# Kernel tuning notes

Measured on AMD Instinct MI355X. Metric: run time of the kernel, lower is better.

## Reference

```python
import jax, jax.numpy as jnp
import numpy as np

COLOR_SIZE = 4
SIZE = 64
FILTERS = 512
LENGTH = SIZE * SIZE * 3  # 12288


def setup_inputs() -> dict:
    key = jax.random.key(0)
    k1, k2, k3 = jax.random.split(key, 3)
    example = jax.random.randint(k1, (8, SIZE, SIZE, 3), 0, COLOR_SIZE, dtype=jnp.int32)
    kernel = jax.random.normal(k2, (FILTERS, LENGTH), dtype=jnp.float32)
    bias = jnp.zeros((FILTERS,), dtype=jnp.float32)
    dense_w = jax.random.normal(k3, (FILTERS, COLOR_SIZE), dtype=jnp.float32) * 0.02
    dense_b = jnp.zeros((COLOR_SIZE,), dtype=jnp.float32)
    return {"example": example, "kernel": kernel, "bias": bias,
            "dense_w": dense_w, "dense_b": dense_b}


def reference(example, kernel, bias, dense_w, dense_b):
    B = example.shape[0]
    L = kernel.shape[1]  # 12288
    # normalize int pixels to [-1, 1)
    x = example.astype(jnp.float32) / COLOR_SIZE * 2.0 - 1.0
    x = x.reshape(B, L)                                   # [B, L]
    # FFT-based long (causal full) convolution, fft_length = 2L
    Xf = jnp.fft.rfft(x, n=2 * L, axis=-1)                # [B, L+1] complex64
    Kf = jnp.fft.rfft(kernel, n=2 * L, axis=-1)           # [F, L+1]
    y = jnp.fft.irfft(Xf[:, None, :] * Kf[None, :, :], n=2 * L, axis=-1)[..., :L]  # [B, F, L]
    y = jnp.transpose(y, (0, 2, 1)) + bias                # [B, L, F]
    y = jax.nn.relu(y)
    out = y @ dense_w + dense_b                           # [B, L, color_size]
    return out.reshape(B, SIZE, SIZE, 3, COLOR_SIZE).astype(jnp.float32)
```

## Files before the change

### kernel.cpp

```cpp
#include <hip/hip_runtime.h>

#define FF 512
#define LL 12288
#define NJC 1556
#define NR 128

typedef _Float16 half8 __attribute__((ext_vector_type(8)));
typedef float    f32x4 __attribute__((ext_vector_type(4)));

__global__ __launch_bounds__(256) void build_At(const float* __restrict__ kern,
                                                _Float16* __restrict__ At) {
    int tid  = blockIdx.x * 256 + threadIdx.x;
    int lane = tid & 63;
    int rest = tid >> 6;
    int dc   = rest % 384;
    int ft   = rest / 384;
    int f    = ft * 16 + (lane & 15);
    int d0   = dc * 32 + (lane >> 4) * 8;
    const float* src = kern + (size_t)f * LL + d0;
    half8 v;
#pragma unroll
    for (int i = 0; i < 8; ++i) v[i] = (_Float16)src[i];
    ((half8*)At)[tid] = v;
}

__global__ __launch_bounds__(256) void build_XB(const int* __restrict__ ex,
                                                _Float16* __restrict__ XB) {
    int tid = blockIdx.x * 256 + threadIdx.x;
    if (tid >= NJC * NR) return;
    int r  = tid & 127;
    int jc = tid >> 7;
    int s  = r >> 3, b = r & 7;
    int j0 = jc * 8;
    half8 v;
#pragma unroll
    for (int i = 0; i < 8; ++i) {
        int idx = LL - 1 - (j0 + i) - s;
        float x = 0.f;
        if (idx >= 0) x = (float)ex[b * LL + idx] * 0.5f - 1.0f;
        v[i] = (_Float16)x;
    }
    ((half8*)XB)[tid] = v;
}

__global__ __launch_bounds__(256) void init_out(const float* __restrict__ db,
                                                float* __restrict__ out) {
    int tid = blockIdx.x * 256 + threadIdx.x;
    out[tid] = db[tid & 3];
}

__device__ __forceinline__ void gl_lds16(const half8* g, half8* l) {
    __builtin_amdgcn_global_load_lds((const __attribute__((address_space(1))) void*)g,
                                     (__attribute__((address_space(3))) void*)l, 16, 0, 0);
}

__global__ __launch_bounds__(256, 2) void conv_main(const _Float16* __restrict__ At,
                                                    const _Float16* __restrict__ XB,
                                                    const float* __restrict__ bias,
                                                    const float* __restrict__ dw,
                                                    float* __restrict__ out) {
    __shared__ half8 Abuf[2][4][8][64];

    int bx    = blockIdx.x;
    int slot  = bx & 7;
    int f_blk = slot >> 1;
    int n_blk = 383 - ((bx >> 3) * 2 + (slot & 1));
    int n0 = n_blk << 5;
    int M  = (n_blk + 4) >> 2;

    int tid  = threadIdx.x;
    int lane = tid & 63;
    int wid  = tid >> 6;
    int quad = lane >> 4;
    int bb   = lane & 7;
    int nh   = (lane >> 3) & 1;

    const half8* Ag  = (const half8*)At;
    const half8* ag0 = Ag + ((size_t)(f_blk * 8 + wid) * 384) * 64 + lane;
    const half8* ag1 = Ag + ((size_t)(f_blk * 8 + wid + 4) * 384) * 64 + lane;

    const half8* Bg = (const half8*)XB;
    int jc0 = 1534 - 4 * n_blk + quad - 2 * nh;
    const half8* pB[4];
#pragma unroll
    for (int t = 0; t < 4; ++t) {
        int tt = wid * 4 + t;
        int r  = (15 - tt) * 8 + bb;
        pB[t] = Bg + (size_t)jc0 * 128 + r;
    }

    f32x4 acc[8][4];
#pragma unroll
    for (int r8 = 0; r8 < 8; ++r8)
#pragma unroll
        for (int t = 0; t < 4; ++t) acc[r8][t] = (f32x4){0.f, 0.f, 0.f, 0.f};

#pragma unroll
    for (int sub = 0; sub < 4; ++sub) {
        gl_lds16(ag0 + (size_t)sub * 64, &Abuf[0][sub][wid][lane]);
        gl_lds16(ag1 + (size_t)sub * 64, &Abuf[0][sub][wid + 4][lane]);
    }
    half8 bcur[4], bnxt[4];
#pragma unroll
    for (int t = 0; t < 4; ++t) bcur[t] = pB[t][0];
    __syncthreads();

    for (int mc = 0; mc < M; ++mc) {
        int buf = mc & 1;
        if (mc + 1 < M) {
            size_t oa = (size_t)(mc + 1) * 256;
#pragma unroll
            for (int sub = 0; sub < 4; ++sub) {
                gl_lds16(ag0 + oa + (size_t)sub * 64, &Abuf[buf ^ 1][sub][wid][lane]);
                gl_lds16(ag1 + oa + (size_t)sub * 64, &Abuf[buf ^ 1][sub][wid + 4][lane]);
            }
        }
#pragma unroll
        for (int sub = 0; sub < 4; ++sub) {
            int dc = mc * 4 + sub;
            size_t ob = (size_t)(dc + 1) * 512;
#pragma unroll
            for (int t = 0; t < 4; ++t) bnxt[t] = pB[t][ob];
            half8 a[8];
#pragma unroll
            for (int r8 = 0; r8 < 8; ++r8) a[r8] = Abuf[buf][sub][r8][lane];
#pragma unroll
            for (int r8 = 0; r8 < 8; ++r8)
#pragma unroll
                for (int t = 0; t < 4; ++t)
                    acc[r8][t] = __builtin_amdgcn_mfma_f32_16x16x32_f16(a[r8], bcur[t], acc[r8][t], 0, 0, 0);
#pragma unroll
            for (int t = 0; t < 4; ++t) bcur[t] = bnxt[t];
        }
        __syncthreads();
    }

    float p[4][4] = {{0.f}};
#pragma unroll
    for (int r8 = 0; r8 < 8; ++r8) {
#pragma unroll
        for (int reg = 0; reg < 4; ++reg) {
            int f = f_blk * 128 + r8 * 16 + quad * 4 + reg;
            float bs = bias[f];
            float4 w = *(const float4*)(dw + (size_t)f * 4);
#pragma unroll
            for (int t = 0; t < 4; ++t) {
                float y = fmaxf(acc[r8][t][reg] + bs, 0.f);
                p[t][0] += y * w.x; p[t][1] += y * w.y;
                p[t][2] += y * w.z; p[t][3] += y * w.w;
            }
        }
    }
#pragma unroll
    for (int t = 0; t < 4; ++t)
#pragma unroll
        for (int c = 0; c < 4; ++c) {
            float v = p[t][c];
            v += __shfl_xor(v, 16, 64);
            v += __shfl_xor(v, 32, 64);
            p[t][c] = v;
        }
    if (quad == 0) {
#pragma unroll
        for (int t = 0; t < 4; ++t) {
            int n = n0 + (wid * 4 + t) + 16 * nh;
            float* o = out + ((size_t)bb * LL + n) * 4;
#pragma unroll
            for (int c = 0; c < 4; ++c) atomicAdd(o + c, p[t][c]);
        }
    }
}

extern "C" void kernel_launch(void* const* d_in, const int* in_sizes, int n_in,
                              void* d_out, int out_size, void* d_ws, size_t ws_size,
                              hipStream_t stream) {
    const int*   ex   = (const int*)d_in[0];
    const float* kern = (const float*)d_in[1];
    const float* bias = (const float*)d_in[2];
    const float* dw   = (const float*)d_in[3];
    const float* db   = (const float*)d_in[4];
    float* out = (float*)d_out;

    _Float16* At = (_Float16*)d_ws;
    _Float16* XB = (_Float16*)((char*)d_ws + (size_t)FF * LL * 2);

    hipLaunchKernelGGL(build_At, dim3(3072), dim3(256), 0, stream, kern, At);
    hipLaunchKernelGGL(build_XB, dim3(778),  dim3(256), 0, stream, ex, XB);
    hipLaunchKernelGGL(init_out, dim3(1536), dim3(256), 0, stream, db, out);
    hipLaunchKernelGGL(conv_main, dim3(1536), dim3(256), 0, stream, At, XB, bias, dw, out);
}
```

Measured before the change: 520.1 us.

## Switch causal-conv GEMM from 16x16x32 to 32x32x16 MFMA tiles

Changes the main Toeplitz-style convolution GEMM to use 32x32x16 f16 MFMA instructions instead of 16x16x32. The A-operand layout produced by build_At, the LDS buffer shape, the B fragment indexing and the epilogue row mapping are all reworked to match the new fragment layout. The aim is fewer MFMA issues and operand fetches per FLOP and better register-level reuse of each A/B fragment. It raises accumulator register pressure (16 floats per tile) and changes the B load pattern, which could affect occupancy or memory coalescing.

```diff
diff --git a/kernel.cpp b/kernel.cpp
--- a/kernel.cpp
+++ b/kernel.cpp
@@ -5,18 +5,18 @@
 #define NJC 1556
 #define NR 128
 
-typedef _Float16 half8 __attribute__((ext_vector_type(8)));
-typedef float    f32x4 __attribute__((ext_vector_type(4)));
+typedef _Float16 half8  __attribute__((ext_vector_type(8)));
+typedef float    f32x16 __attribute__((ext_vector_type(16)));
 
 __global__ __launch_bounds__(256) void build_At(const float* __restrict__ kern,
                                                 _Float16* __restrict__ At) {
     int tid  = blockIdx.x * 256 + threadIdx.x;
     int lane = tid & 63;
     int rest = tid >> 6;
-    int dc   = rest % 384;
-    int ft   = rest / 384;
-    int f    = ft * 16 + (lane & 15);
-    int d0   = dc * 32 + (lane >> 4) * 8;
+    int kc   = rest % 768;
+    int ft   = rest / 768;
+    int f    = ft * 32 + (lane & 31);
+    int d0   = kc * 16 + (lane >> 5) * 8;
     const float* src = kern + (size_t)f * LL + d0;
     half8 v;
 #pragma unroll
@@ -59,114 +59,126 @@
                                                     const float* __restrict__ bias,
                                                     const float* __restrict__ dw,
                                                     float* __restrict__ out) {
-    __shared__ half8 Abuf[2][4][8][64];
+    __shared__ half8 Abuf[2][8][4][64];
 
     int bx    = blockIdx.x;
     int slot  = bx & 7;
     int f_blk = slot >> 1;
     int n_blk = 383 - ((bx >> 3) * 2 + (slot & 1));
     int n0 = n_blk << 5;
-    int M  = (n_blk + 4) >> 2;
+    int S  = n_blk + 1;
+    int M  = (S + 3) >> 2;
 
     int tid  = threadIdx.x;
     int lane = tid & 63;
     int wid  = tid >> 6;
-    int quad = lane >> 4;
+    int kh   = lane >> 5;
     int bb   = lane & 7;
-    int nh   = (lane >> 3) & 1;
-
-    const half8* Ag  = (const half8*)At;
-    const half8* ag0 = Ag + ((size_t)(f_blk * 8 + wid) * 384) * 64 + lane;
-    const half8* ag1 = Ag + ((size_t)(f_blk * 8 + wid + 4) * 384) * 64 + lane;
+    int nh   = (lane >> 3) & 3;
+
+    const half8* Ag = (const half8*)At;
+    const half8* ag = Ag + ((size_t)(f_blk * 4 + wid) * 768) * 64 + lane;
 
     const half8* Bg = (const half8*)XB;
-    int jc0 = 1534 - 4 * n_blk + quad - 2 * nh;
-    const half8* pB[4];
-#pragma unroll
-    for (int t = 0; t < 4; ++t) {
-        int tt = wid * 4 + t;
-        int r  = (15 - tt) * 8 + bb;
-        pB[t] = Bg + (size_t)jc0 * 128 + r;
-    }
-
-    f32x4 acc[8][4];
-#pragma unroll
-    for (int r8 = 0; r8 < 8; ++r8)
-#pragma unroll
-        for (int t = 0; t < 4; ++t) acc[r8][t] = (f32x4){0.f, 0.f, 0.f, 0.f};
-
-#pragma unroll
-    for (int sub = 0; sub < 4; ++sub) {
-        gl_lds16(ag0 + (size_t)sub * 64, &Abuf[0][sub][wid][lane]);
-        gl_lds16(ag1 + (size_t)sub * 64, &Abuf[0][sub][wid + 4][lane]);
-    }
-    half8 bcur[4], bnxt[4];
-#pragma unroll
-    for (int t = 0; t < 4; ++t) bcur[t] = pB[t][0];
+    const half8* pB[2];
+#pragma unroll
+    for (int ti = 0; ti < 2; ++ti) {
+        int n_base = n0 + (wid * 2 + ti) * 4;
+        int Qt = LL - 1 - n_base - nh;
+        int s  = Qt & 7;
+        int jc0 = Qt >> 3;
+        pB[ti] = Bg + (size_t)(jc0 + kh) * 128 + s * 8 + bb;
+    }
+
+    f32x16 acc[4][2];
+#pragma unroll
+    for (int mt = 0; mt < 4; ++mt)
+#pragma unroll
+        for (int ti = 0; ti < 2; ++ti)
+#pragma unroll
+            for (int r = 0; r < 16; ++r) acc[mt][ti][r] = 0.f;
+
+#pragma unroll
+    for (int kc = 0; kc < 8; ++kc)
+        gl_lds16(ag + (size_t)kc * 64, &Abuf[0][kc][wid][lane]);
+    half8 bf[2][2][2];
+#pragma unroll
+    for (int ti = 0; ti < 2; ++ti) {
+        bf[0][0][ti] = pB[ti][0];
+        bf[0][1][ti] = pB[ti][256];
+    }
     __syncthreads();
 
     for (int mc = 0; mc < M; ++mc) {
         int buf = mc & 1;
         if (mc + 1 < M) {
-            size_t oa = (size_t)(mc + 1) * 256;
-#pragma unroll
-            for (int sub = 0; sub < 4; ++sub) {
-                gl_lds16(ag0 + oa + (size_t)sub * 64, &Abuf[buf ^ 1][sub][wid][lane]);
-                gl_lds16(ag1 + oa + (size_t)sub * 64, &Abuf[buf ^ 1][sub][wid + 4][lane]);
+            size_t oa = (size_t)(mc + 1) * 512;
+#pragma unroll
+            for (int kc = 0; kc < 8; ++kc)
+                gl_lds16(ag + oa + (size_t)kc * 64, &Abuf[buf ^ 1][kc][wid][lane]);
+        }
+#pragma unroll
+        for (int d4 = 0; d4 < 4; ++d4) {
+            int dcg = mc * 4 + d4;
+            int p   = dcg & 1;
+            size_t ob = (size_t)(dcg + 1) * 512;
+#pragma unroll
+            for (int ti = 0; ti < 2; ++ti) {
+                bf[p ^ 1][0][ti] = pB[ti][ob];
+                bf[p ^ 1][1][ti] = pB[ti][ob + 256];
             }
-        }
-#pragma unroll
-        for (int sub = 0; sub < 4; ++sub) {
-            int dc = mc * 4 + sub;
-            size_t ob = (size_t)(dc + 1) * 512;
-#pragma unroll
-            for (int t = 0; t < 4; ++t) bnxt[t] = pB[t][ob];
-            half8 a[8];
-#pragma unroll
-            for (int r8 = 0; r8 < 8; ++r8) a[r8] = Abuf[buf][sub][r8][lane];
-#pragma unroll
-            for (int r8 = 0; r8 < 8; ++r8)
-#pragma unroll
-                for (int t = 0; t < 4; ++t)
-                    acc[r8][t] = __builtin_amdgcn_mfma_f32_16x16x32_f16(a[r8], bcur[t], acc[r8][t], 0, 0, 0);
-#pragma unroll
-            for (int t = 0; t < 4; ++t) bcur[t] = bnxt[t];
+            half8 a0[4], a1[4];
+#pragma unroll
+            for (int mt = 0; mt < 4; ++mt) {
+                a0[mt] = Abuf[buf][d4 * 2][mt][lane];
+                a1[mt] = Abuf[buf][d4 * 2 + 1][mt][lane];
+            }
+#pragma unroll
+            for (int mt = 0; mt < 4; ++mt)
+#pragma unroll
+                for (int ti = 0; ti < 2; ++ti)
+                    acc[mt][ti] = __builtin_amdgcn_mfma_f32_32x32x16_f16(a0[mt], bf[p][0][ti], acc[mt][ti], 0, 0, 0);
+#pragma unroll
+            for (int mt = 0; mt < 4; ++mt)
+#pragma unroll
+                for (int ti = 0; ti < 2; ++ti)
+                    acc[mt][ti] = __builtin_amdgcn_mfma_f32_32x32x16_f16(a1[mt], bf[p][1][ti], acc[mt][ti], 0, 0, 0);
         }
         __syncthreads();
     }
 
-    float p[4][4] = {{0.f}};
-#pragma unroll
-    for (int r8 = 0; r8 < 8; ++r8) {
-#pragma unroll
-        for (int reg = 0; reg < 4; ++reg) {
-            int f = f_blk * 128 + r8 * 16 + quad * 4 + reg;
+    float p[2][4] = {{0.f}};
+#pragma unroll
+    for (int mt = 0; mt < 4; ++mt) {
+#pragma unroll
+        for (int reg = 0; reg < 16; ++reg) {
+            int row = (reg & 3) + 8 * (reg >> 2) + 4 * kh;
+            int f   = f_blk * 128 + mt * 32 + row;
             float bs = bias[f];
             float4 w = *(const float4*)(dw + (size_t)f * 4);
 #pragma unroll
-            for (int t = 0; t < 4; ++t) {
-                float y = fmaxf(acc[r8][t][reg] + bs, 0.f);
-                p[t][0] += y * w.x; p[t][1] += y * w.y;
-                p[t][2] += y * w.z; p[t][3] += y * w.w;
+            for (int ti = 0; ti < 2; ++ti) {
+                float y = fmaxf(acc[mt][ti][reg] + bs, 0.f);
+                p[ti][0] += y * w.x; p[ti][1] += y * w.y;
+                p[ti][2] += y * w.z; p[ti][3] += y * w.w;
             }
         }
     }
 #pragma unroll
-    for (int t = 0; t < 4; ++t)
+    for (int ti = 0; ti < 2; ++ti)
 #pragma unroll
         for (int c = 0; c < 4; ++c) {
-            float v = p[t][c];
-            v += __shfl_xor(v, 16, 64);
+            float v = p[ti][c];
             v += __shfl_xor(v, 32, 64);
-            p[t][c] = v;
-        }
-    if (quad == 0) {
-#pragma unroll
-        for (int t = 0; t < 4; ++t) {
-            int n = n0 + (wid * 4 + t) + 16 * nh;
+            p[ti][c] = v;
+        }
+    if (kh == 0) {
+#pragma unroll
+        for (int ti = 0; ti < 2; ++ti) {
+            int n = n0 + (wid * 2 + ti) * 4 + nh;
             float* o = out + ((size_t)bb * LL + n) * 4;
 #pragma unroll
-            for (int c = 0; c < 4; ++c) atomicAdd(o + c, p[t][c]);
+            for (int c = 0; c < 4; ++c) atomicAdd(o + c, p[ti][c]);
         }
     }
 }
```

After: 550.0 us. 5.8% more time.
